# Kernel optimization log

Hardware: AMD Instinct MI355X
Metric: run time of the kernel (lower is better)

## Reference

```python
import jax, jax.numpy as jnp
import numpy as np

B, R, N = 4, 1024, 100
REG_FG_THRESH = 0.55
EPS = 1e-8


def _cross2(a, b):
    return a[..., 0] * b[..., 1] - a[..., 1] * b[..., 0]


def _corners_bev(box):
    # box: (7,) [x,y,z,dx,dy,dz,heading] -> (4,2) CCW BEV corners
    x, y, dx, dy, ang = box[0], box[1], box[3], box[4], box[6]
    c, s = jnp.cos(ang), jnp.sin(ang)
    lx = jnp.array([0.5, -0.5, -0.5, 0.5], dtype=box.dtype) * dx
    ly = jnp.array([0.5, 0.5, -0.5, -0.5], dtype=box.dtype) * dy
    return jnp.stack([x + lx * c - ly * s, y + lx * s + ly * c], axis=-1)


def _points_in_box(pts, box):
    # pts (P,2), box (7,) -> (P,) bool; transform into box frame
    c, s = jnp.cos(box[6]), jnp.sin(box[6])
    px = pts[:, 0] - box[0]
    py = pts[:, 1] - box[1]
    lx = px * c + py * s
    ly = -px * s + py * c
    return (jnp.abs(lx) <= box[3] * 0.5 + 1e-5) & (jnp.abs(ly) <= box[4] * 0.5 + 1e-5)


def _bev_inter_area(boxa, boxb):
    # exact rotated-rectangle intersection area (convex polygon of <=8 verts)
    ca = _corners_bev(boxa)
    cb = _corners_bev(boxb)
    in_b = _points_in_box(ca, boxb)
    in_a = _points_in_box(cb, boxa)
    a1, a2 = ca, jnp.roll(ca, -1, axis=0)
    b1, b2 = cb, jnp.roll(cb, -1, axis=0)
    d1 = a2 - a1
    d2 = b2 - b1
    denom = _cross2(d1[:, None, :], d2[None, :, :])              # (4,4)
    diff = b1[None, :, :] - a1[:, None, :]                       # (4,4,2)
    safe = jnp.where(jnp.abs(denom) > EPS, denom, EPS)
    t = _cross2(diff, d2[None, :, :]) / safe
    u = _cross2(diff, d1[:, None, :]) / safe
    hit = (jnp.abs(denom) > EPS) & (t >= 0) & (t <= 1) & (u >= 0) & (u <= 1)
    pin = a1[:, None, :] + t[..., None] * d1[:, None, :]         # (4,4,2)
    pts = jnp.concatenate([ca, cb, pin.reshape(16, 2)], axis=0)  # (24,2)
    val = jnp.concatenate([in_b, in_a, hit.reshape(16)], axis=0)
    nv = val.sum()
    ctr = (pts * val[:, None]).sum(0) / jnp.maximum(nv, 1)
    ang = jnp.where(val, jnp.arctan2(pts[:, 1] - ctr[1], pts[:, 0] - ctr[0]), 1e9)
    order = jnp.argsort(ang)
    p = pts[order]
    v = val[order]
    first = p[0]
    p = jnp.where(v[:, None], p, first)   # pad invalid slots with first vertex (zero shoelace contribution)
    q = jnp.roll(p, -1, axis=0)
    area = 0.5 * jnp.abs(jnp.sum(p[:, 0] * q[:, 1] - q[:, 0] * p[:, 1]))
    return jnp.where(nv >= 3, area, jnp.zeros((), dtype=pts.dtype))


def _iou3d_pair(a, b):
    # same math as iou3d_nms_utils.boxes_iou3d_gpu for one pair
    inter_bev = _bev_inter_area(a, b)
    oh = jnp.clip(jnp.minimum(a[2] + a[5] * 0.5, b[2] + b[5] * 0.5)
                  - jnp.maximum(a[2] - a[5] * 0.5, b[2] - b[5] * 0.5), 0.0)
    inter = inter_bev * oh
    va = a[3] * a[4] * a[5]
    vb = b[3] * b[4] * b[5]
    return inter / jnp.clip(va + vb - inter, 1e-6, None)


_iou_rois_gts = jax.vmap(jax.vmap(_iou3d_pair, in_axes=(None, 0)), in_axes=(0, None))  # (R,N)
_iou_batched = jax.vmap(_iou_rois_gts)                                                  # (B,R,N)


def setup_inputs() -> dict:
    key = jax.random.key(0)
    ks = jax.random.split(key, 9)
    xy = jax.random.uniform(ks[0], (B, N, 2), minval=-40.0, maxval=40.0)
    z = jax.random.uniform(ks[1], (B, N, 1), minval=-2.0, maxval=0.0)
    dims = jax.random.uniform(ks[2], (B, N, 3), minval=1.0, maxval=4.5)
    heading = jax.random.uniform(ks[3], (B, N, 1), minval=-np.pi, maxval=np.pi)
    labels = jax.random.randint(ks[4], (B, N, 1), 1, 4).astype(jnp.float32)
    gt_boxes = jnp.concatenate([xy, z, dims, heading, labels], axis=-1)  # (B,N,8)
    # sampling ROIs are jittered GT boxes, mirroring generate_sampling_roi
    base_idx = jax.random.randint(ks[5], (B, R), 0, N)
    base = jnp.take_along_axis(gt_boxes[..., :7], base_idx[..., None], axis=1)  # (B,R,7)
    ctr_off = jax.random.uniform(ks[6], (B, R, 3), minval=-0.5, maxval=0.5) * base[..., 3:6]
    scale = jax.random.uniform(ks[7], (B, R, 3), minval=0.8, maxval=1.25)
    ang_off = jax.random.uniform(ks[8], (B, R, 1), minval=-np.pi / 4, maxval=np.pi / 4)
    sampling_rois = jnp.concatenate(
        [base[..., :3] + ctr_off, base[..., 3:6] * scale, base[..., 6:7] + ang_off], axis=-1)
    sampling_rois_labels = jnp.take_along_axis(gt_boxes[..., 7], base_idx, axis=1).astype(jnp.int32)
    return {"sampling_rois": sampling_rois,
            "sampling_rois_labels": sampling_rois_labels,
            "gt_boxes": gt_boxes}


def reference(sampling_rois, sampling_rois_labels, gt_boxes):
    # sample_rois_for_rcnn core: all-pairs rotated 3D IoU, best-GT assignment,
    # gather gt_of_rois, then forward()'s reg_valid_mask thresholding.
    iou3d = _iou_batched(sampling_rois, gt_boxes[..., :7])        # (B,R,N)
    max_overlaps = iou3d.max(axis=-1)                             # (B,R)
    gt_assignment = iou3d.argmax(axis=-1)                         # (B,R)
    gt_of_rois = jnp.take_along_axis(gt_boxes, gt_assignment[..., None], axis=1)  # (B,R,8)
    reg_valid_mask = (max_overlaps > REG_FG_THRESH).astype(jnp.int32)
    return sampling_rois, gt_of_rois, max_overlaps, sampling_rois_labels, reg_valid_mask
```

## Files before the change

kernel.cpp:

```cpp
#include <hip/hip_runtime.h>
#include <math.h>

#define BB 4
#define RR 1024
#define NN 100
#define NROI (BB * RR)

#define INIT_PACK 0x00000000FFFFFFFFull

__device__ __forceinline__ void corner_of(int i, float cx0, float cy0, float dx, float dy,
                                          float c, float s, float& X, float& Y) {
    float sx = (i == 0 || i == 3) ? 0.5f : -0.5f;
    float sy = (i <= 1) ? 0.5f : -0.5f;
    float lx = sx * dx, ly = sy * dy;
    X = cx0 + lx * c - ly * s;
    Y = cy0 + lx * s + ly * c;
}

__global__ __launch_bounds__(256) void sampling_target_wave(
    const float* __restrict__ rois,
    const int*   __restrict__ labels,
    const float* __restrict__ gts,
    float*       __restrict__ out)
{
    const int r    = (int)((blockIdx.x * blockDim.x + threadIdx.x) >> 6);
    const int lane = threadIdx.x & 63;
    if (r >= NROI) return;
    const int b = r >> 10;
    const float* gbase = gts + b * NN * 8;

    const float* A = rois + r * 7;
    const float ax = A[0], ay = A[1], az = A[2];
    const float adx = A[3], ady = A[4], adz = A[5], aang = A[6];
    const float ra   = 0.5f * sqrtf(adx * adx + ady * ady);
    const float azlo = az - adz * 0.5f, azhi = az + adz * 0.5f;

    unsigned long long m0, m1;
    {
        unsigned long long mm[2];
#pragma unroll
        for (int it = 0; it < 2; it++) {
            int n = it * 64 + lane;
            bool pass = false;
            if (n < NN) {
                const float* G = gbase + n * 8;
                float gx = G[0], gy = G[1], gz = G[2];
                float gdx = G[3], gdy = G[4], gdz = G[5];
                float oh = fminf(azhi, gz + gdz * 0.5f) - fmaxf(azlo, gz - gdz * 0.5f);
                float dxc = ax - gx, dyc = ay - gy;
                float rb = 0.5f * sqrtf(gdx * gdx + gdy * gdy);
                float rr = ra + rb;
                pass = (oh > 0.0f) && (dxc * dxc + dyc * dyc <= rr * rr);
            }
            mm[it] = __ballot(pass);
        }
        m0 = mm[0]; m1 = mm[1];
    }

    const float acs = cosf(aang), asn = sinf(aang);
    const int half = lane >> 5;
    const int l32  = lane & 31;

    unsigned long long best = INIT_PACK;

    while (m0 | m1) {
        int na, nb = -1;
        if (m0) { na = __ffsll((unsigned long long)m0) - 1;      m0 &= m0 - 1; }
        else    { na = __ffsll((unsigned long long)m1) - 1 + 64; m1 &= m1 - 1; }
        if (m0)      { nb = __ffsll((unsigned long long)m0) - 1;      m0 &= m0 - 1; }
        else if (m1) { nb = __ffsll((unsigned long long)m1) - 1 + 64; m1 &= m1 - 1; }

        const int  myN    = half ? nb : na;
        const bool active = (myN >= 0);
        const float* G = gbase + (active ? myN : 0) * 8;
        float gx = G[0], gy = G[1], gz = G[2];
        float gdx = G[3], gdy = G[4], gdz = G[5], gang = G[6];
        float bcs = cosf(gang), bsn = sinf(gang);

        float ppx = 0.0f, ppy = 0.0f;
        bool val = false;
        if (l32 < 4) {
            corner_of(l32, ax, ay, adx, ady, acs, asn, ppx, ppy);
            float qx = ppx - gx, qy = ppy - gy;
            float lx = qx * bcs + qy * bsn;
            float ly = -qx * bsn + qy * bcs;
            val = (fabsf(lx) <= gdx * 0.5f + 1e-5f) && (fabsf(ly) <= gdy * 0.5f + 1e-5f);
        } else if (l32 < 8) {
            corner_of(l32 - 4, gx, gy, gdx, gdy, bcs, bsn, ppx, ppy);
            float qx = ppx - ax, qy = ppy - ay;
            float lx = qx * acs + qy * asn;
            float ly = -qx * asn + qy * acs;
            val = (fabsf(lx) <= adx * 0.5f + 1e-5f) && (fabsf(ly) <= ady * 0.5f + 1e-5f);
        } else if (l32 < 24) {
            int e = l32 - 8, ii = e >> 2, jj = e & 3;
            float a1x, a1y, a2x, a2y, b1x, b1y, b2x, b2y;
            corner_of(ii, ax, ay, adx, ady, acs, asn, a1x, a1y);
            corner_of((ii + 1) & 3, ax, ay, adx, ady, acs, asn, a2x, a2y);
            corner_of(jj, gx, gy, gdx, gdy, bcs, bsn, b1x, b1y);
            corner_of((jj + 1) & 3, gx, gy, gdx, gdy, bcs, bsn, b2x, b2y);
            float d1x = a2x - a1x, d1y = a2y - a1y;
            float d2x = b2x - b1x, d2y = b2y - b1y;
            float denom = d1x * d2y - d1y * d2x;
            float fx = b1x - a1x, fy = b1y - a1y;
            float safe = (fabsf(denom) > 1e-8f) ? denom : 1e-8f;
            float t = (fx * d2y - fy * d2x) / safe;
            float u = (fx * d1y - fy * d1x) / safe;
            ppx = a1x + t * d1x;
            ppy = a1y + t * d1y;
            val = (fabsf(denom) > 1e-8f) && (t >= 0.0f) && (t <= 1.0f) && (u >= 0.0f) && (u <= 1.0f);
        }
        val = val && active;

        unsigned long long bm = __ballot(val);
        unsigned gm = half ? (unsigned)(bm >> 32) : (unsigned)(bm & 0xFFFFFFFFull);
        int nv = __popc(gm);

        float inter_bev = 0.0f;
        if (nv >= 3) {
            float sx = val ? ppx : 0.0f;
            float sy = val ? ppy : 0.0f;
#pragma unroll
            for (int off = 16; off; off >>= 1) {
                sx += __shfl_xor(sx, off, 32);
                sy += __shfl_xor(sy, off, 32);
            }
            float cx = sx / (float)nv, cy = sy / (float)nv;

            float myAng = val ? atan2f(ppy - cy, ppx - cx) : 1e9f;

            float sAng = 1e30f; int sIdx = 0; bool found = false;
            float gAng = 1e30f; int gIdx = 0;
#pragma unroll
            for (int j = 0; j < 24; j++) {
                float aj = __shfl(myAng, j, 32);
                if (aj < 1e8f) {
                    bool greater = (aj > myAng) || (aj == myAng && j > l32);
                    if (greater && aj < sAng) { sAng = aj; sIdx = j; found = true; }
                    if (aj < gAng) { gAng = aj; gIdx = j; }
                }
            }
            int qi = found ? sIdx : gIdx;
            float qx = __shfl(ppx, qi, 32);
            float qy = __shfl(ppy, qi, 32);
            float contrib = val ? (ppx * qy - qx * ppy) : 0.0f;
#pragma unroll
            for (int off = 16; off; off >>= 1)
                contrib += __shfl_xor(contrib, off, 32);
            inter_bev = 0.5f * fabsf(contrib);
        }

        if (active) {
            float oh = fminf(azhi, gz + gdz * 0.5f) - fmaxf(azlo, gz - gdz * 0.5f);
            float inter = inter_bev * oh;
            float va = adx * ady * adz;
            float vb = gdx * gdy * gdz;
            float v = inter / fmaxf(va + vb - inter, 1e-6f);
            unsigned long long packed =
                ((unsigned long long)__float_as_uint(v) << 32) | (unsigned)(~(unsigned)myN);
            best = (packed > best) ? packed : best;
        }
    }

    {
        unsigned long long other = __shfl(best, lane ^ 32, 64);
        best = (other > best) ? other : best;
    }

    float mo = __uint_as_float((unsigned)(best >> 32));
    int besti = (int)(~(unsigned)(best & 0xFFFFFFFFu));

    float* out_rois = out;
    float* out_gor  = out + NROI * 7;
    float* out_max  = out_gor + NROI * 8;
    float* out_lab  = out_max + NROI;
    float* out_msk  = out_lab + NROI;

    if (lane < 7) {
        out_rois[r * 7 + lane] = A[lane];
    } else if (lane < 15) {
        int k = lane - 7;
        out_gor[r * 8 + k] = gbase[besti * 8 + k];
    } else if (lane == 15) {
        out_max[r] = mo;
    } else if (lane == 16) {
        out_lab[r] = (float)labels[r];
    } else if (lane == 17) {
        out_msk[r] = (mo > 0.55f) ? 1.0f : 0.0f;
    }
}

extern "C" void kernel_launch(void* const* d_in, const int* in_sizes, int n_in,
                              void* d_out, int out_size, void* d_ws, size_t ws_size,
                              hipStream_t stream) {
    const float* rois   = (const float*)d_in[0];
    const int*   labels = (const int*)d_in[1];
    const float* gts    = (const float*)d_in[2];
    float* out = (float*)d_out;

    hipLaunchKernelGGL(sampling_target_wave, dim3(NROI / 4), dim3(256), 0, stream,
                       rois, labels, gts, out);
}
```

Before: 72.71 us.

## Precompute per-box trig, corners and bounds in a separate prepass kernel

Adds a precompute kernel that writes each GT box's and ROI's cos/sin, BEV corners, half-extents, z-range, radius and volume into workspace, with GT fields stored structure-of-arrays. The evaluation kernel then loads these values instead of recomputing trig and corners in every pair iteration and in every lane. This removes repeated transcendental and corner arithmetic from the inner loop. In exchange it adds a second kernel launch and more scattered global/L2 loads per iteration.

```diff
diff --git a/kernel.cpp b/kernel.cpp
--- a/kernel.cpp
+++ b/kernel.cpp
@@ -5,6 +5,9 @@
 #define RR 1024
 #define NN 100
 #define NROI (BB * RR)
+
+#define GT_F (18 * NN)
+#define ROI_OFF (BB * GT_F)
 
 #define INIT_PACK 0x00000000FFFFFFFFull
 
@@ -17,23 +20,78 @@
     Y = cy0 + lx * s + ly * c;
 }
 
-__global__ __launch_bounds__(256) void sampling_target_wave(
+__global__ __launch_bounds__(256) void precompute_kernel(
+    const float* __restrict__ rois, const float* __restrict__ gts,
+    float* __restrict__ ws)
+{
+    int t = blockIdx.x * blockDim.x + threadIdx.x;
+    if (t < BB * NN) {
+        int b = t / NN, n = t - b * NN;
+        const float4* gp = (const float4*)(gts + t * 8);
+        float4 g0 = gp[0];
+        float4 g1 = gp[1];
+        float gx = g0.x, gy = g0.y, gz = g0.z, gdx = g0.w;
+        float gdy = g1.x, gdz = g1.y, gang = g1.z;
+        float c = cosf(gang), s = sinf(gang);
+        float* T = ws + b * GT_F;
+        T[0 * NN + n] = gx;
+        T[1 * NN + n] = gy;
+        T[2 * NN + n] = gz - gdz * 0.5f;
+        T[3 * NN + n] = gz + gdz * 0.5f;
+        T[4 * NN + n] = 0.5f * sqrtf(gdx * gdx + gdy * gdy);
+        T[5 * NN + n] = c;
+        T[6 * NN + n] = s;
+        T[7 * NN + n] = gdx * 0.5f + 1e-5f;
+        T[8 * NN + n] = gdy * 0.5f + 1e-5f;
+        T[9 * NN + n] = gdx * gdy * gdz;
+#pragma unroll
+        for (int i = 0; i < 4; i++) {
+            float X, Y;
+            corner_of(i, gx, gy, gdx, gdy, c, s, X, Y);
+            T[(10 + i) * NN + n] = X;
+            T[(14 + i) * NN + n] = Y;
+        }
+    } else if (t < BB * NN + NROI) {
+        int r = t - BB * NN;
+        const float* A = rois + r * 7;
+        float ax = A[0], ay = A[1], az = A[2];
+        float adx = A[3], ady = A[4], adz = A[5], aang = A[6];
+        float c = cosf(aang), s = sinf(aang);
+        float* Rt = ws + ROI_OFF + r * 20;
+        Rt[0] = ax; Rt[1] = ay;
+        Rt[2] = az - adz * 0.5f;
+        Rt[3] = az + adz * 0.5f;
+        Rt[4] = 0.5f * sqrtf(adx * adx + ady * ady);
+        Rt[5] = c; Rt[6] = s;
+        Rt[7] = adx * 0.5f + 1e-5f;
+        Rt[8] = ady * 0.5f + 1e-5f;
+        Rt[9] = adx * ady * adz;
+#pragma unroll
+        for (int i = 0; i < 4; i++) {
+            float X, Y;
+            corner_of(i, ax, ay, adx, ady, c, s, X, Y);
+            Rt[10 + i] = X;
+            Rt[14 + i] = Y;
+        }
+    }
+}
+
+__global__ __launch_bounds__(256) void eval_kernel(
     const float* __restrict__ rois,
     const int*   __restrict__ labels,
     const float* __restrict__ gts,
+    const float* __restrict__ ws,
     float*       __restrict__ out)
 {
     const int r    = (int)((blockIdx.x * blockDim.x + threadIdx.x) >> 6);
     const int lane = threadIdx.x & 63;
     if (r >= NROI) return;
     const int b = r >> 10;
-    const float* gbase = gts + b * NN * 8;
-
-    const float* A = rois + r * 7;
-    const float ax = A[0], ay = A[1], az = A[2];
-    const float adx = A[3], ady = A[4], adz = A[5], aang = A[6];
-    const float ra   = 0.5f * sqrtf(adx * adx + ady * ady);
-    const float azlo = az - adz * 0.5f, azhi = az + adz * 0.5f;
+    const float* T  = ws + b * GT_F;
+    const float* Rt = ws + ROI_OFF + r * 20;
+
+    const float ax = Rt[0], ay = Rt[1], azlo = Rt[2], azhi = Rt[3], ara = Rt[4];
+    const float acs = Rt[5], asn = Rt[6], ahx = Rt[7], ahy = Rt[8], va = Rt[9];
 
     unsigned long long m0, m1;
     {
@@ -43,13 +101,9 @@
             int n = it * 64 + lane;
             bool pass = false;
             if (n < NN) {
-                const float* G = gbase + n * 8;
-                float gx = G[0], gy = G[1], gz = G[2];
-                float gdx = G[3], gdy = G[4], gdz = G[5];
-                float oh = fminf(azhi, gz + gdz * 0.5f) - fmaxf(azlo, gz - gdz * 0.5f);
-                float dxc = ax - gx, dyc = ay - gy;
-                float rb = 0.5f * sqrtf(gdx * gdx + gdy * gdy);
-                float rr = ra + rb;
+                float oh = fminf(azhi, T[3 * NN + n]) - fmaxf(azlo, T[2 * NN + n]);
+                float dxc = ax - T[0 * NN + n], dyc = ay - T[1 * NN + n];
+                float rr = ara + T[4 * NN + n];
                 pass = (oh > 0.0f) && (dxc * dxc + dyc * dyc <= rr * rr);
             }
             mm[it] = __ballot(pass);
@@ -57,47 +111,45 @@
         m0 = mm[0]; m1 = mm[1];
     }
 
-    const float acs = cosf(aang), asn = sinf(aang);
     const int half = lane >> 5;
     const int l32  = lane & 31;
-
     unsigned long long best = INIT_PACK;
 
     while (m0 | m1) {
         int na, nb = -1;
-        if (m0) { na = __ffsll((unsigned long long)m0) - 1;      m0 &= m0 - 1; }
-        else    { na = __ffsll((unsigned long long)m1) - 1 + 64; m1 &= m1 - 1; }
-        if (m0)      { nb = __ffsll((unsigned long long)m0) - 1;      m0 &= m0 - 1; }
-        else if (m1) { nb = __ffsll((unsigned long long)m1) - 1 + 64; m1 &= m1 - 1; }
+        if (m0) { na = __ffsll(m0) - 1;      m0 &= m0 - 1; }
+        else    { na = __ffsll(m1) - 1 + 64; m1 &= m1 - 1; }
+        if (m0)      { nb = __ffsll(m0) - 1;      m0 &= m0 - 1; }
+        else if (m1) { nb = __ffsll(m1) - 1 + 64; m1 &= m1 - 1; }
 
         const int  myN    = half ? nb : na;
         const bool active = (myN >= 0);
-        const float* G = gbase + (active ? myN : 0) * 8;
-        float gx = G[0], gy = G[1], gz = G[2];
-        float gdx = G[3], gdy = G[4], gdz = G[5], gang = G[6];
-        float bcs = cosf(gang), bsn = sinf(gang);
+        const int  nn     = active ? myN : 0;
+        float gx  = T[0 * NN + nn], gy  = T[1 * NN + nn];
+        float bcs = T[5 * NN + nn], bsn = T[6 * NN + nn];
+        float bhx = T[7 * NN + nn], bhy = T[8 * NN + nn];
 
         float ppx = 0.0f, ppy = 0.0f;
         bool val = false;
         if (l32 < 4) {
-            corner_of(l32, ax, ay, adx, ady, acs, asn, ppx, ppy);
+            ppx = Rt[10 + l32]; ppy = Rt[14 + l32];
             float qx = ppx - gx, qy = ppy - gy;
             float lx = qx * bcs + qy * bsn;
             float ly = -qx * bsn + qy * bcs;
-            val = (fabsf(lx) <= gdx * 0.5f + 1e-5f) && (fabsf(ly) <= gdy * 0.5f + 1e-5f);
+            val = (fabsf(lx) <= bhx) && (fabsf(ly) <= bhy);
         } else if (l32 < 8) {
-            corner_of(l32 - 4, gx, gy, gdx, gdy, bcs, bsn, ppx, ppy);
+            int i4 = l32 - 4;
+            ppx = T[(10 + i4) * NN + nn]; ppy = T[(14 + i4) * NN + nn];
             float qx = ppx - ax, qy = ppy - ay;
             float lx = qx * acs + qy * asn;
             float ly = -qx * asn + qy * acs;
-            val = (fabsf(lx) <= adx * 0.5f + 1e-5f) && (fabsf(ly) <= ady * 0.5f + 1e-5f);
+            val = (fabsf(lx) <= ahx) && (fabsf(ly) <= ahy);
         } else if (l32 < 24) {
             int e = l32 - 8, ii = e >> 2, jj = e & 3;
-            float a1x, a1y, a2x, a2y, b1x, b1y, b2x, b2y;
-            corner_of(ii, ax, ay, adx, ady, acs, asn, a1x, a1y);
-            corner_of((ii + 1) & 3, ax, ay, adx, ady, acs, asn, a2x, a2y);
-            corner_of(jj, gx, gy, gdx, gdy, bcs, bsn, b1x, b1y);
-            corner_of((jj + 1) & 3, gx, gy, gdx, gdy, bcs, bsn, b2x, b2y);
+            float a1x = Rt[10 + ii],          a1y = Rt[14 + ii];
+            float a2x = Rt[10 + ((ii+1)&3)],  a2y = Rt[14 + ((ii+1)&3)];
+            float b1x = T[(10 + jj) * NN + nn],        b1y = T[(14 + jj) * NN + nn];
+            float b2x = T[(10 + ((jj+1)&3)) * NN + nn], b2y = T[(14 + ((jj+1)&3)) * NN + nn];
             float d1x = a2x - a1x, d1y = a2y - a1y;
             float d2x = b2x - b1x, d2y = b2y - b1y;
             float denom = d1x * d2y - d1y * d2x;
@@ -150,11 +202,9 @@
         }
 
         if (active) {
-            float oh = fminf(azhi, gz + gdz * 0.5f) - fmaxf(azlo, gz - gdz * 0.5f);
+            float oh = fminf(azhi, T[3 * NN + nn]) - fmaxf(azlo, T[2 * NN + nn]);
             float inter = inter_bev * oh;
-            float va = adx * ady * adz;
-            float vb = gdx * gdy * gdz;
-            float v = inter / fmaxf(va + vb - inter, 1e-6f);
+            float v = inter / fmaxf(va + T[9 * NN + nn] - inter, 1e-6f);
             unsigned long long packed =
                 ((unsigned long long)__float_as_uint(v) << 32) | (unsigned)(~(unsigned)myN);
             best = (packed > best) ? packed : best;
@@ -176,10 +226,10 @@
     float* out_msk  = out_lab + NROI;
 
     if (lane < 7) {
-        out_rois[r * 7 + lane] = A[lane];
+        out_rois[r * 7 + lane] = rois[r * 7 + lane];
     } else if (lane < 15) {
         int k = lane - 7;
-        out_gor[r * 8 + k] = gbase[besti * 8 + k];
+        out_gor[r * 8 + k] = gts[(b * NN + besti) * 8 + k];
     } else if (lane == 15) {
         out_max[r] = mo;
     } else if (lane == 16) {
@@ -196,7 +246,11 @@
     const int*   labels = (const int*)d_in[1];
     const float* gts    = (const float*)d_in[2];
     float* out = (float*)d_out;
-
-    hipLaunchKernelGGL(sampling_target_wave, dim3(NROI / 4), dim3(256), 0, stream,
-                       rois, labels, gts, out);
-}
+    float* ws  = (float*)d_ws;
+
+    int k1_threads = BB * NN + NROI;
+    hipLaunchKernelGGL(precompute_kernel, dim3((k1_threads + 255) / 256), dim3(256), 0, stream,
+                       rois, gts, ws);
+    hipLaunchKernelGGL(eval_kernel, dim3(NROI / 4), dim3(256), 0, stream,
+                       rois, labels, gts, ws, out);
+}
```

After: 72.15 us. No clear change (-0.8%).
